# Kernel tuning notes

Measured on AMD Instinct MI355X. Metric: run time of the kernel, lower is better.

The kernel has to match this reference:

```python
import jax, jax.numpy as jnp
import numpy as np

N_NODES = 50000
N_EDGES = 800000
IN_FEATS = 256
OUT_FEATS = 128
NEG_SLOPE = 0.2


def setup_inputs() -> dict:
    key = jax.random.key(0)
    k1, k2, k3, k4 = jax.random.split(key, 4)
    feat = jax.random.normal(k1, (N_NODES, IN_FEATS), dtype=jnp.float32)
    limit = float(np.sqrt(6.0 / (IN_FEATS + OUT_FEATS)))  # xavier_uniform
    W = jax.random.uniform(k2, (IN_FEATS, OUT_FEATS), dtype=jnp.float32,
                           minval=-limit, maxval=limit)
    bias = jnp.zeros((OUT_FEATS,), dtype=jnp.float32)
    src = jax.random.randint(k3, (N_EDGES,), 0, N_NODES, dtype=jnp.int64)
    dst = jax.random.randint(k4, (N_EDGES,), 0, N_NODES, dtype=jnp.int64)
    return {"feat": feat, "W": W, "bias": bias, "src": src, "dst": dst}


def reference(feat, W, bias, src, dst):
    N = feat.shape[0]
    ones = jnp.ones(src.shape[0], dtype=feat.dtype)
    # degrees (clamped to 1, as in the torch code)
    out_deg = jnp.maximum(jax.ops.segment_sum(ones, src, num_segments=N), 1.0)
    in_deg = jnp.maximum(jax.ops.segment_sum(ones, dst, num_segments=N), 1.0)
    # norm == 'both': pre-scale by out-degree^-1/2
    h = feat * (out_deg ** -0.5)[:, None]
    # in_feats > out_feats branch: project first
    h = h @ W  # [N, out_feats]
    hs = h[src]          # [E, out_feats] gather
    hd = jnp.tanh(h[dst])  # [E, out_feats] gather
    e = jnp.sum(hs * hd, axis=1)                      # [E]
    e = jnp.where(e > 0, e, NEG_SLOPE * e)            # leaky_relu(0.2)
    # edge_softmax: softmax over edges grouped by destination node
    emax = jax.ops.segment_max(e, dst, num_segments=N)
    emax = jnp.where(jnp.isfinite(emax), emax, 0.0)   # guard empty groups
    ee = jnp.exp(e - emax[dst])
    esum = jax.ops.segment_sum(ee, dst, num_segments=N)
    e_soft = ee / esum[dst]
    # update_all(copy_u, sum): unweighted scatter-sum of src features into dst
    rst = jax.ops.segment_sum(hs, dst, num_segments=N)  # [N, out_feats]
    # norm == 'both': post-scale by in-degree^-1/2, then bias (activation=None)
    rst = rst * (in_deg ** -0.5)[:, None] + bias
    return rst, e_soft
```

## Files before the change

kernel.cpp:

```cpp
#include <hip/hip_runtime.h>
#include <math.h>

#define NNODES 50000
#define NEDGES 800000
#define INFEAT 256
#define OUTF   128
#define NEG_SLOPE 0.2f
#define MAXDEG 64
#define GBM 64
#define GEMM_NB 782
#define HB 128
#define HW 12500

typedef __attribute__((ext_vector_type(8))) short bf16x8;
typedef __attribute__((ext_vector_type(4))) float f32x4;

__device__ __forceinline__ ushort f2bf(float f) {
    unsigned u = __float_as_uint(f);
    unsigned r = (u + 0x7FFFu + ((u >> 16) & 1u)) >> 16;
    return (ushort)r;
}
__device__ __forceinline__ float bflo(unsigned u) { return __uint_as_float(u << 16); }
__device__ __forceinline__ float bfhi(unsigned u) { return __uint_as_float(u & 0xFFFF0000u); }

__global__ void kwbt(const float* __restrict__ W, ushort* __restrict__ whi,
                     ushort* __restrict__ wlo) {
    int i = blockIdx.x * 256 + threadIdx.x;
    int n = i >> 8, k = i & 255;
    float w = W[(size_t)k * OUTF + n];
    ushort h = f2bf(w);
    float hf = __uint_as_float((unsigned)h << 16);
    whi[i] = h;
    wlo[i] = f2bf(w - hf);
}

__launch_bounds__(256)
__global__ void kfused(const float* __restrict__ feat, const uint4* __restrict__ whi,
                       const uint4* __restrict__ wlo, unsigned* __restrict__ hb,
                       const int* __restrict__ src, const int* __restrict__ dst,
                       int* __restrict__ fill, int* __restrict__ ebd,
                       unsigned* __restrict__ hist_part, int M, int E) {
    __shared__ unsigned sh[HW + 300];
    int tid = threadIdx.x;

    if (blockIdx.x < HB) {
        for (int j = tid; j < HW; j += 256) sh[j] = 0;
        __syncthreads();
        for (int i = blockIdx.x * 256 + tid; i < E; i += HB * 256) {
            int s = src[i];
            atomicAdd(&sh[s >> 2], 1u << ((s & 3) * 8));
        }
        __syncthreads();
        unsigned* gp = hist_part + (size_t)blockIdx.x * HW;
        for (int j = tid; j < HW; j += 256) gp[j] = sh[j];
        return;
    }

    int b2 = blockIdx.x - HB;
    if (b2 & 1) {
        for (int i = (b2 >> 1) * 256 + tid; i < E; i += GEMM_NB * 256) {
            int d = dst[i];
            int p = atomicAdd(&fill[d], 1);
            if (p < MAXDEG) ebd[(d << 6) + p] = i;
        }
        return;
    }

    uint4* Bh = (uint4*)sh;
    uint4* Bo = Bh + 1024;
    int lane = tid & 63, wid = tid >> 6;
    int gb = b2 >> 1;

    int m0 = gb * GBM + wid * 16;
    int arow = m0 + (lane & 15);
    int ar = arow < M ? arow : M - 1;
    const float* ap = &feat[(size_t)ar * INFEAT + ((lane >> 4) << 3)];

    union { uint4 u; bf16x8 s; } ahi[8], alo[8];
    #pragma unroll
    for (int ks = 0; ks < 8; ks++) {
        float4 a0 = *(const float4*)&ap[ks * 32];
        float4 a1 = *(const float4*)&ap[ks * 32 + 4];
        float av[8] = {a0.x, a0.y, a0.z, a0.w, a1.x, a1.y, a1.z, a1.w};
        unsigned hw[4], lw[4];
        #pragma unroll
        for (int q = 0; q < 4; q++) {
            asm("v_cvt_pk_bf16_f32 %0, %1, %2" : "=v"(hw[q]) : "v"(av[2*q]), "v"(av[2*q+1]));
            float h0 = bflo(hw[q]);
            float h1 = bfhi(hw[q]);
            float l0 = av[2*q] - h0;
            float l1 = av[2*q+1] - h1;
            asm("v_cvt_pk_bf16_f32 %0, %1, %2" : "=v"(lw[q]) : "v"(l0), "v"(l1));
        }
        ahi[ks].u = make_uint4(hw[0], hw[1], hw[2], hw[3]);
        alo[ks].u = make_uint4(lw[0], lw[1], lw[2], lw[3]);
    }

    f32x4 acc[8];
    #pragma unroll
    for (int i = 0; i < 8; i++) acc[i] = (f32x4){0.f, 0.f, 0.f, 0.f};

    #pragma unroll
    for (int h = 0; h < 4; h++) {
        __syncthreads();
        #pragma unroll
        for (int r = 0; r < 4; r++) {
            int g = tid + 256 * r;
            int nl = g >> 5, kc = g & 31;
            int gi = (h * 32 + nl) * 32 + kc;
            int li = (nl << 5) | (kc ^ (nl & 7));
            Bh[li] = whi[gi];
            Bo[li] = wlo[gi];
        }
        __syncthreads();
        #pragma unroll
        for (int ks = 0; ks < 8; ks++) {
            int kcb = (ks << 2) + (lane >> 4);
            #pragma unroll
            for (int nt = 0; nt < 2; nt++) {
                int nl = (nt << 4) | (lane & 15);
                int li = (nl << 5) | (kcb ^ (nl & 7));
                union { uint4 u; bf16x8 s; } bh, bo;
                bh.u = Bh[li];
                bo.u = Bo[li];
                int ai = h * 2 + nt;
                acc[ai] = __builtin_amdgcn_mfma_f32_16x16x32_bf16(ahi[ks].s, bh.s, acc[ai], 0, 0, 0);
                acc[ai] = __builtin_amdgcn_mfma_f32_16x16x32_bf16(alo[ks].s, bh.s, acc[ai], 0, 0, 0);
                acc[ai] = __builtin_amdgcn_mfma_f32_16x16x32_bf16(ahi[ks].s, bo.s, acc[ai], 0, 0, 0);
            }
        }
    }

    #pragma unroll
    for (int ai = 0; ai < 8; ai++) {
        #pragma unroll
        for (int q = 0; q < 4; q++) {
            float v = acc[ai][q];
            float vp = __shfl_xor(v, 1, 64);
            int grow = m0 + ((lane >> 4) << 2) + q;
            if (!(lane & 1) && grow < M) {
                unsigned w;
                asm("v_cvt_pk_bf16_f32 %0, %1, %2" : "=v"(w) : "v"(v), "v"(vp));
                hb[(size_t)grow * 64 + ((ai << 4) | (lane & 15)) / 2] = w;
            }
        }
    }
}

__global__ void kred(const unsigned* __restrict__ hist_part, int* __restrict__ cnt_out) {
    int j = blockIdx.x * 256 + threadIdx.x;
    if (j >= HW) return;
    unsigned a01 = 0, a23 = 0;
    for (int b = 0; b < HB; b++) {
        unsigned v = hist_part[(size_t)b * HW + j];
        a01 += v & 0x00FF00FFu;
        a23 += (v >> 8) & 0x00FF00FFu;
    }
    int n = j * 4;
    cnt_out[n]     = (int)(a01 & 0xFFFFu);
    cnt_out[n + 1] = (int)(a23 & 0xFFFFu);
    cnt_out[n + 2] = (int)(a01 >> 16);
    cnt_out[n + 3] = (int)(a23 >> 16);
}

__device__ __forceinline__ void agg_node(int n, float* thlw,
                                         const unsigned* __restrict__ hb,
                                         const int* __restrict__ src,
                                         const int* __restrict__ ebd,
                                         const int* __restrict__ fill,
                                         const int* __restrict__ cnt_out,
                                         const float* __restrict__ bias,
                                         float* __restrict__ out_rst,
                                         float* __restrict__ out_es) {
    int lane = threadIdx.x & 63;
    int deg = fill[n];
    if (deg > MAXDEG) deg = MAXDEG;
    const int ROWU = OUTF / 2;

    int g = lane >> 3;
    int t = lane & 7;
    int c = t * 16;

    {
        int co = cnt_out[n];
        float sc_d = rsqrtf((float)(co < 1 ? 1 : co));
        unsigned u = hb[(size_t)n * ROWU + lane];
        thlw[2 * lane]     = tanhf(sc_d * bflo(u));
        thlw[2 * lane + 1] = tanhf(sc_d * bfhi(u));
    }
    float thf[16];
    #pragma unroll
    for (int q = 0; q < 4; q++) {
        float4 v = *(float4*)&thlw[c + q * 4];
        thf[q*4+0] = v.x; thf[q*4+1] = v.y; thf[q*4+2] = v.z; thf[q*4+3] = v.w;
    }

    int eid = 0, s = 0;
    if (lane < deg) { eid = ebd[(n << 6) + lane]; s = src[eid]; }

    float accf[16];
    #pragma unroll
    for (int k = 0; k < 16; k++) accf[k] = 0.f;
    float myv = -INFINITY;

    for (int base = 0; base < deg; base += 8) {
        int m = base + g;
        int sj = __shfl(s, m, 64);
        uint4 r0 = make_uint4(0u, 0u, 0u, 0u), r1 = r0;
        float scs = 0.f;
        if (m < deg) {
            const uint4* rp = (const uint4*)&hb[(size_t)sj * ROWU + t * 8];
            r0 = rp[0]; r1 = rp[1];
            int co = cnt_out[sj];
            scs = rsqrtf((float)(co < 1 ? 1 : co));
        }
        unsigned ua[8] = {r0.x, r0.y, r0.z, r0.w, r1.x, r1.y, r1.z, r1.w};
        float pd = 0.f;
        #pragma unroll
        for (int k = 0; k < 8; k++) {
            float lo = bflo(ua[k]), hi = bfhi(ua[k]);
            accf[2*k]   = fmaf(scs, lo, accf[2*k]);
            accf[2*k+1] = fmaf(scs, hi, accf[2*k+1]);
            pd += lo * thf[2*k] + hi * thf[2*k+1];
        }
        #pragma unroll
        for (int msk = 1; msk < 8; msk <<= 1) pd += __shfl_xor(pd, msk, 64);
        float p = scs * pd;
        float e = p > 0.f ? p : NEG_SLOPE * p;
        if (m < deg && t == (base >> 3)) myv = e;
    }

    if (deg > 0) {
        float mx = myv;
        #pragma unroll
        for (int msk = 1; msk < 64; msk <<= 1) mx = fmaxf(mx, __shfl_xor(mx, msk, 64));
        int m = 8 * t + g;
        float v = (m < deg) ? expf(myv - mx) : 0.f;
        float sum = v;
        #pragma unroll
        for (int msk = 1; msk < 64; msk <<= 1) sum += __shfl_xor(sum, msk, 64);
        float inv = 1.f / sum;
        int eidm = __shfl(eid, m, 64);
        if (m < deg) out_es[eidm] = v * inv;
    }

    #pragma unroll
    for (int msk = 8; msk < 64; msk <<= 1) {
        #pragma unroll
        for (int k = 0; k < 16; k++) accf[k] += __shfl_xor(accf[k], msk, 64);
    }
    if (g == 0) {
        float sc = rsqrtf((float)(deg < 1 ? 1 : deg));
        #pragma unroll
        for (int q = 0; q < 4; q++) {
            float4 b = *(const float4*)&bias[c + q * 4];
            float4 r = make_float4(accf[4*q]   * sc + b.x, accf[4*q+1] * sc + b.y,
                                   accf[4*q+2] * sc + b.z, accf[4*q+3] * sc + b.w);
            *(float4*)&out_rst[(size_t)n * OUTF + c + q * 4] = r;
        }
    }
}

__launch_bounds__(256)
__global__ void kagg(const unsigned* __restrict__ hb, const int* __restrict__ src,
                     const int* __restrict__ ebd, const int* __restrict__ fill,
                     const int* __restrict__ cnt_out, const float* __restrict__ bias,
                     float* __restrict__ out_rst, float* __restrict__ out_es,
                     int nnodes) {
    __shared__ float thl[4][128];
    int wid = threadIdx.x >> 6;
    int n = blockIdx.x * 4 + wid;
    if (n >= nnodes) return;
    agg_node(n, &thl[wid][0], hb, src, ebd, fill, cnt_out, bias, out_rst, out_es);
}

extern "C" void kernel_launch(void* const* d_in, const int* in_sizes, int n_in,
                              void* d_out, int out_size, void* d_ws, size_t ws_size,
                              hipStream_t stream) {
    const float* feat = (const float*)d_in[0];
    const float* W    = (const float*)d_in[1];
    const float* bias = (const float*)d_in[2];
    const int*   src  = (const int*)d_in[3];
    const int*   dst  = (const int*)d_in[4];

    float* out_rst = (float*)d_out;
    float* out_es  = (float*)d_out + (size_t)NNODES * OUTF;

    char* ws = (char*)d_ws;
    size_t o = 0;
    auto alloc = [&](size_t bytes) { void* p = ws + o; o += (bytes + 255) & ~(size_t)255; return p; };
    int*      cnt_out   = (int*)alloc(NNODES * 4);
    int*      fill      = (int*)alloc(NNODES * 4);
    int*      ebd       = (int*)alloc((size_t)NNODES * MAXDEG * 4);
    ushort*   whi       = (ushort*)alloc((size_t)OUTF * INFEAT * 2);
    ushort*   wlo       = (ushort*)alloc((size_t)OUTF * INFEAT * 2);
    ushort*   hb        = (ushort*)alloc((size_t)NNODES * OUTF * 2);
    unsigned* hist_part = (unsigned*)alloc((size_t)HB * HW * 4);
    (void)o; (void)ws_size; (void)in_sizes; (void)n_in; (void)out_size;

    hipMemsetAsync(fill, 0, NNODES * 4, stream);

    kwbt<<<(OUTF * INFEAT + 255) / 256, 256, 0, stream>>>(W, whi, wlo);

    kfused<<<HB + 2 * GEMM_NB, 256, 0, stream>>>(feat, (const uint4*)whi, (const uint4*)wlo,
                                                 (unsigned*)hb, src, dst,
                                                 fill, ebd, hist_part, NNODES, NEDGES);

    kred<<<(HW + 255) / 256, 256, 0, stream>>>(hist_part, cnt_out);

    kagg<<<(NNODES + 3) / 4, 256, 0, stream>>>((const unsigned*)hb, src, ebd, fill,
                                               cnt_out, bias, out_rst, out_es, NNODES);
}
```

Baseline: 117.8 us.

## Replace global atomic bucket fill with per-slice dst histograms and prefix bases

Instead of global atomicAdd on a per-node fill counter to bucket edges by destination, the code now builds per-slice dst histograms (8-bit packed counters) alongside src histograms, prefix-sums them per slice, and has each bucket block assign slots with LDS atomics seeded from the slice base. This removes the global atomic contention and the memset, and reuses the hb/ebd buffers as scratch for histograms. The cost is an extra pass over dst and a serial prefix loop over 128 slices. Packed 8-bit counts can overflow if a node's in-degree exceeds 255.

```diff
diff --git a/kernel.cpp b/kernel.cpp
--- a/kernel.cpp
+++ b/kernel.cpp
@@ -9,7 +9,8 @@
 #define MAXDEG 64
 #define GBM 64
 #define GEMM_NB 782
-#define HB 128
+#define NSLICE 128
+#define EPS 6250
 #define HW 12500
 
 typedef __attribute__((ext_vector_type(8))) short bf16x8;
@@ -23,45 +24,96 @@
 __device__ __forceinline__ float bflo(unsigned u) { return __uint_as_float(u << 16); }
 __device__ __forceinline__ float bfhi(unsigned u) { return __uint_as_float(u & 0xFFFF0000u); }
 
-__global__ void kwbt(const float* __restrict__ W, ushort* __restrict__ whi,
-                     ushort* __restrict__ wlo) {
-    int i = blockIdx.x * 256 + threadIdx.x;
+__launch_bounds__(256)
+__global__ void kprep(const int* __restrict__ src, const int* __restrict__ dst,
+                      const float* __restrict__ W,
+                      unsigned* __restrict__ hist_src, unsigned* __restrict__ hist_dst,
+                      ushort* __restrict__ whi, ushort* __restrict__ wlo, int E) {
+    __shared__ unsigned sh[HW];
+    int tid = threadIdx.x;
+    if (blockIdx.x < 2 * NSLICE) {
+        const int* arr = (blockIdx.x < NSLICE) ? src : dst;
+        unsigned* out = (blockIdx.x < NSLICE) ? hist_src : hist_dst;
+        int slice = blockIdx.x & (NSLICE - 1);
+        for (int j = tid; j < HW; j += 256) sh[j] = 0;
+        __syncthreads();
+        int e0 = slice * EPS, e1 = e0 + EPS;
+        for (int i = e0 + tid; i < e1; i += 256) {
+            int a = arr[i];
+            atomicAdd(&sh[a >> 2], 1u << ((a & 3) * 8));
+        }
+        __syncthreads();
+        unsigned* gp = out + (size_t)slice * HW;
+        for (int j = tid; j < HW; j += 256) gp[j] = sh[j];
+        return;
+    }
+    int i = (blockIdx.x - 2 * NSLICE) * 256 + tid;
     int n = i >> 8, k = i & 255;
     float w = W[(size_t)k * OUTF + n];
     ushort h = f2bf(w);
-    float hf = __uint_as_float((unsigned)h << 16);
     whi[i] = h;
-    wlo[i] = f2bf(w - hf);
+    wlo[i] = f2bf(w - __uint_as_float((unsigned)h << 16));
+}
+
+__launch_bounds__(256)
+__global__ void kred(const unsigned* __restrict__ hist_src,
+                     const unsigned* __restrict__ hist_dst,
+                     int* __restrict__ cnt_out, unsigned* __restrict__ basepart,
+                     int* __restrict__ indeg) {
+    if (blockIdx.x < 49) {
+        int j = blockIdx.x * 256 + threadIdx.x;
+        if (j >= HW) return;
+        unsigned a01 = 0, a23 = 0;
+        for (int s = 0; s < NSLICE; s++) {
+            unsigned v = hist_src[(size_t)s * HW + j];
+            a01 += v & 0x00FF00FFu;
+            a23 += (v >> 8) & 0x00FF00FFu;
+        }
+        int n = j * 4;
+        cnt_out[n]     = (int)(a01 & 0xFFFFu);
+        cnt_out[n + 1] = (int)(a23 & 0xFFFFu);
+        cnt_out[n + 2] = (int)(a01 >> 16);
+        cnt_out[n + 3] = (int)(a23 >> 16);
+        return;
+    }
+    int j = (blockIdx.x - 49) * 256 + threadIdx.x;
+    if (j >= HW) return;
+    unsigned run = 0;
+    for (int s = 0; s < NSLICE; s++) {
+        basepart[(size_t)s * HW + j] = run;
+        run += hist_dst[(size_t)s * HW + j];
+    }
+    int n = j * 4;
+    indeg[n]     = (int)(run & 0xFFu);
+    indeg[n + 1] = (int)((run >> 8) & 0xFFu);
+    indeg[n + 2] = (int)((run >> 16) & 0xFFu);
+    indeg[n + 3] = (int)(run >> 24);
 }
 
 __launch_bounds__(256)
 __global__ void kfused(const float* __restrict__ feat, const uint4* __restrict__ whi,
                        const uint4* __restrict__ wlo, unsigned* __restrict__ hb,
-                       const int* __restrict__ src, const int* __restrict__ dst,
-                       int* __restrict__ fill, int* __restrict__ ebd,
-                       unsigned* __restrict__ hist_part, int M, int E) {
-    __shared__ unsigned sh[HW + 300];
+                       const int* __restrict__ dst, const unsigned* __restrict__ basepart,
+                       int* __restrict__ ebd, int M, int E) {
+    __shared__ unsigned sh[8192];
     int tid = threadIdx.x;
 
-    if (blockIdx.x < HB) {
-        for (int j = tid; j < HW; j += 256) sh[j] = 0;
-        __syncthreads();
-        for (int i = blockIdx.x * 256 + tid; i < E; i += HB * 256) {
-            int s = src[i];
-            atomicAdd(&sh[s >> 2], 1u << ((s & 3) * 8));
-        }
-        __syncthreads();
-        unsigned* gp = hist_part + (size_t)blockIdx.x * HW;
-        for (int j = tid; j < HW; j += 256) gp[j] = sh[j];
-        return;
-    }
-
-    int b2 = blockIdx.x - HB;
-    if (b2 & 1) {
-        for (int i = (b2 >> 1) * 256 + tid; i < E; i += GEMM_NB * 256) {
+    if (blockIdx.x < 512 && (blockIdx.x & 1)) {
+        int bb = blockIdx.x >> 1;
+        int slice = bb >> 1, half = bb & 1;
+        int nb0 = half * (HW / 2);
+        for (int w = tid; w < HW / 2; w += 256)
+            sh[w] = basepart[(size_t)slice * HW + nb0 + w];
+        __syncthreads();
+        int d0 = half * 25000, e0 = slice * EPS, e1 = e0 + EPS;
+        for (int i = e0 + tid; i < e1; i += 256) {
             int d = dst[i];
-            int p = atomicAdd(&fill[d], 1);
-            if (p < MAXDEG) ebd[(d << 6) + p] = i;
+            int ld = d - d0;
+            if ((unsigned)ld < 25000u) {
+                unsigned old = atomicAdd(&sh[ld >> 2], 1u << ((ld & 3) * 8));
+                int p = (int)((old >> ((ld & 3) * 8)) & 0xFFu);
+                if (p < MAXDEG) ebd[(d << 6) + p] = i;
+            }
         }
         return;
     }
@@ -69,7 +121,7 @@
     uint4* Bh = (uint4*)sh;
     uint4* Bo = Bh + 1024;
     int lane = tid & 63, wid = tid >> 6;
-    int gb = b2 >> 1;
+    int gb = (blockIdx.x < 512) ? (blockIdx.x >> 1) : (blockIdx.x - 256);
 
     int m0 = gb * GBM + wid * 16;
     int arow = m0 + (lane & 15);
@@ -147,33 +199,17 @@
     }
 }
 
-__global__ void kred(const unsigned* __restrict__ hist_part, int* __restrict__ cnt_out) {
-    int j = blockIdx.x * 256 + threadIdx.x;
-    if (j >= HW) return;
-    unsigned a01 = 0, a23 = 0;
-    for (int b = 0; b < HB; b++) {
-        unsigned v = hist_part[(size_t)b * HW + j];
-        a01 += v & 0x00FF00FFu;
-        a23 += (v >> 8) & 0x00FF00FFu;
-    }
-    int n = j * 4;
-    cnt_out[n]     = (int)(a01 & 0xFFFFu);
-    cnt_out[n + 1] = (int)(a23 & 0xFFFFu);
-    cnt_out[n + 2] = (int)(a01 >> 16);
-    cnt_out[n + 3] = (int)(a23 >> 16);
-}
-
 __device__ __forceinline__ void agg_node(int n, float* thlw,
                                          const unsigned* __restrict__ hb,
                                          const int* __restrict__ src,
                                          const int* __restrict__ ebd,
-                                         const int* __restrict__ fill,
+                                         const int* __restrict__ indeg,
                                          const int* __restrict__ cnt_out,
                                          const float* __restrict__ bias,
                                          float* __restrict__ out_rst,
                                          float* __restrict__ out_es) {
     int lane = threadIdx.x & 63;
-    int deg = fill[n];
+    int deg = indeg[n];
     if (deg > MAXDEG) deg = MAXDEG;
     const int ROWU = OUTF / 2;
 
@@ -263,7 +299,7 @@
 
 __launch_bounds__(256)
 __global__ void kagg(const unsigned* __restrict__ hb, const int* __restrict__ src,
-                     const int* __restrict__ ebd, const int* __restrict__ fill,
+                     const int* __restrict__ ebd, const int* __restrict__ indeg,
                      const int* __restrict__ cnt_out, const float* __restrict__ bias,
                      float* __restrict__ out_rst, float* __restrict__ out_es,
                      int nnodes) {
@@ -271,7 +307,7 @@
     int wid = threadIdx.x >> 6;
     int n = blockIdx.x * 4 + wid;
     if (n >= nnodes) return;
-    agg_node(n, &thl[wid][0], hb, src, ebd, fill, cnt_out, bias, out_rst, out_es);
+    agg_node(n, &thl[wid][0], hb, src, ebd, indeg, cnt_out, bias, out_rst, out_es);
 }
 
 extern "C" void kernel_launch(void* const* d_in, const int* in_sizes, int n_in,
@@ -289,25 +325,26 @@
     char* ws = (char*)d_ws;
     size_t o = 0;
     auto alloc = [&](size_t bytes) { void* p = ws + o; o += (bytes + 255) & ~(size_t)255; return p; };
-    int*      cnt_out   = (int*)alloc(NNODES * 4);
-    int*      fill      = (int*)alloc(NNODES * 4);
-    int*      ebd       = (int*)alloc((size_t)NNODES * MAXDEG * 4);
-    ushort*   whi       = (ushort*)alloc((size_t)OUTF * INFEAT * 2);
-    ushort*   wlo       = (ushort*)alloc((size_t)OUTF * INFEAT * 2);
-    ushort*   hb        = (ushort*)alloc((size_t)NNODES * OUTF * 2);
-    unsigned* hist_part = (unsigned*)alloc((size_t)HB * HW * 4);
+    int*      cnt_out  = (int*)alloc(NNODES * 4);
+    int*      indeg    = (int*)alloc(NNODES * 4);
+    int*      ebd      = (int*)alloc((size_t)NNODES * MAXDEG * 4);
+    ushort*   whi      = (ushort*)alloc((size_t)OUTF * INFEAT * 2);
+    ushort*   wlo      = (ushort*)alloc((size_t)OUTF * INFEAT * 2);
+    ushort*   hb       = (ushort*)alloc((size_t)NNODES * OUTF * 2);
+    unsigned* basepart = (unsigned*)alloc((size_t)NSLICE * HW * 4);
+    unsigned* hist_src = (unsigned*)hb;
+    unsigned* hist_dst = (unsigned*)ebd;
     (void)o; (void)ws_size; (void)in_sizes; (void)n_in; (void)out_size;
 
-    hipMemsetAsync(fill, 0, NNODES * 4, stream);
-
-    kwbt<<<(OUTF * INFEAT + 255) / 256, 256, 0, stream>>>(W, whi, wlo);
-
-    kfused<<<HB + 2 * GEMM_NB, 256, 0, stream>>>(feat, (const uint4*)whi, (const uint4*)wlo,
-                                                 (unsigned*)hb, src, dst,
-                                                 fill, ebd, hist_part, NNODES, NEDGES);
-
-    kred<<<(HW + 255) / 256, 256, 0, stream>>>(hist_part, cnt_out);
-
-    kagg<<<(NNODES + 3) / 4, 256, 0, stream>>>((const unsigned*)hb, src, ebd, fill,
+    kprep<<<2 * NSLICE + 128, 256, 0, stream>>>(src, dst, W, hist_src, hist_dst,
+                                                whi, wlo, NEDGES);
+
+    kred<<<98, 256, 0, stream>>>(hist_src, hist_dst, cnt_out, basepart, indeg);
+
+    kfused<<<GEMM_NB + 256, 256, 0, stream>>>(feat, (const uint4*)whi, (const uint4*)wlo,
+                                              (unsigned*)hb, dst, basepart, ebd,
+                                              NNODES, NEDGES);
+
+    kagg<<<(NNODES + 3) / 4, 256, 0, stream>>>((const unsigned*)hb, src, ebd, indeg,
                                                cnt_out, bias, out_rst, out_es, NNODES);
 }
```

Result: faster. 112.8 us (-4.2%).
